# Performance work log

Hardware: AMD Instinct MI355X
Metric: run time of the kernel (lower is better)

Reference implementation:

```python
import jax, jax.numpy as jnp
import numpy as np

B, C, N = 4, 1, 1048576  # batch, channels (==spatial_dim==1), grid points
H = 32                   # correction_hidden
DX = 1.0                 # grid spacing


def setup_inputs() -> dict:
    key = jax.random.key(0)
    ks = jax.random.split(key, 4)
    u = jax.random.normal(ks[0], (B, C, N), dtype=jnp.float32)
    # correction MLP params (Linear 1->32, 32->32, 32->1). Original zero-inits
    # the last layer; we use small random values so the correction path is
    # numerically non-trivial for kernel correctness testing.
    W1 = jax.random.normal(ks[1], (1, H), dtype=jnp.float32) * 0.1
    b1 = jnp.zeros((H,), dtype=jnp.float32)
    W2 = jax.random.normal(ks[2], (H, H), dtype=jnp.float32) * 0.1
    b2 = jnp.zeros((H,), dtype=jnp.float32)
    W3 = jax.random.normal(ks[3], (H, 1), dtype=jnp.float32) * 0.1
    b3 = jnp.zeros((1,), dtype=jnp.float32)
    return dict(u=u, W1=W1, b1=b1, W2=W2, b2=b2, W3=W3, b3=b3)


def reference(u, W1, b1, W2, b2, W3, b3):
    # FD Laplacian via 1D stencil [1, -2, 1] with zero padding (== conv1d pad=1),
    # then / dx^2.  u: (B, C, N)
    up = jnp.pad(u, ((0, 0), (0, 0), (1, 1)))
    lap = (up[..., :-2] - 2.0 * u + up[..., 2:]) / (DX * DX)
    # correction MLP on per-point features (B, N, C)
    x = jnp.transpose(u, (0, 2, 1))           # (B, N, 1)
    h = jnp.tanh(x @ W1 + b1)                 # (B, N, 32)
    h = jnp.tanh(h @ W2 + b2)                 # (B, N, 32)
    corr = h @ W3 + b3                        # (B, N, 1)
    corr = jnp.transpose(corr, (0, 2, 1)).reshape(u.shape)  # (B, C, N)
    return lap + corr
```

## Files before the change

kernel.cpp:

```cpp
#include <hip/hip_runtime.h>
#include <hip/hip_bf16.h>
#include <math.h>

#define TBL_N       1024
#define TBL_LO      (-10.0f)
#define TBL_HI      (10.0f)
#define TBL_ENTRIES (TBL_N + 2)
#define ROW_N       1048576

__global__ __launch_bounds__(256)
void build_table(const float* __restrict__ c0, const float* __restrict__ c1,
                 const float* __restrict__ c2, const float* __restrict__ c3,
                 const float* __restrict__ W2, const float* __restrict__ b3,
                 float* __restrict__ tbl_g) {
    const int tid  = blockIdx.x * 256 + threadIdx.x;
    const int wave = tid >> 6;
    const int half = (threadIdx.x >> 5) & 1;
    const int j    = threadIdx.x & 31;

    const float a0 = c0[j], a1 = c1[j], a2 = c2[j], a3 = c3[j];
    const int m = (__ballot(a0 != 0.0f) ? 1 : 0) |
                  (__ballot(a1 != 0.0f) ? 2 : 0) |
                  (__ballot(a2 != 0.0f) ? 4 : 0) |
                  (__ballot(a3 != 0.0f) ? 8 : 0);
    float w1 = a0, bb1 = a1, bb2 = a2, w3 = a3;
    if (__popc(m) == 2) {
        const float cand[4] = {a0, a1, a2, a3};
        int f = 0; while (!((m >> f) & 1)) ++f;
        int s = f + 1; while (!((m >> s) & 1)) ++s;
        w1 = cand[f]; w3 = cand[s]; bb1 = 0.0f; bb2 = 0.0f;
    }

    const int e = wave * 2 + half;
    if (e >= TBL_ENTRIES) return;
    const int  en = (e > TBL_N) ? TBL_N : e;
    const float h = (TBL_HI - TBL_LO) / (float)TBL_N;
    const float x = TBL_LO + h * (float)en;

    float h1 = tanhf(fmaf(x, w1, bb1));

    float acc = bb2;
#pragma unroll
    for (int i = 0; i < 32; ++i)
        acc = fmaf(__shfl(h1, i, 32), W2[i * 32 + j], acc);

    float p = tanhf(acc) * w3;
#pragma unroll
    for (int off = 16; off; off >>= 1)
        p += __shfl_down(p, off, 32);

    if (j == 0) tbl_g[e] = p + b3[0];
}

__global__ __launch_bounds__(256)
void hybrid_main(const float* __restrict__ u, float* __restrict__ out,
                 const float* __restrict__ tbl_g, int total) {
    __shared__ float tbl[TBL_ENTRIES];
    for (int k = threadIdx.x; k < TBL_ENTRIES; k += 256)
        tbl[k] = tbl_g[k];
    __syncthreads();

    const float scale = (float)TBL_N / (TBL_HI - TBL_LO);
    const float bias  = -TBL_LO * scale;
    const float tmax  = (float)TBL_N - 0.001f;
    const int nch     = total >> 3;
    const int stride  = gridDim.x * blockDim.x;

    for (int c = blockIdx.x * blockDim.x + threadIdx.x; c < nch; c += stride) {
        const int g  = c << 3;
        const int i0 = g & (ROW_N - 1);
        const float4 p0 = *(const float4*)(u + g);
        const float4 p1 = *(const float4*)(u + g + 4);
        const float v[8] = {p0.x, p0.y, p0.z, p0.w, p1.x, p1.y, p1.z, p1.w};

        const bool atL = (i0 == 0);
        const bool atR = (i0 + 8 == ROW_N);
        float left  = u[atL ? g : g - 1];
        float right = u[atR ? g + 7 : g + 8];
        left  = atL ? 0.0f : left;
        right = atR ? 0.0f : right;

        float r[8];
#pragma unroll
        for (int k = 0; k < 8; ++k) {
            const float lm = (k == 0) ? left  : v[k - 1];
            const float rp = (k == 7) ? right : v[k + 1];
            float t = fmaf(v[k], scale, bias);
            t = fminf(fmaxf(t, 0.0f), tmax);
            const int   ki = (int)t;
            const float fr = t - (float)ki;
            const float f0 = tbl[ki];
            const float f1 = tbl[ki + 1];
            r[k] = (lm + rp) - 2.0f * v[k] + fmaf(f1 - f0, fr, f0);
        }

        *(float4*)(out + g)     = make_float4(r[0], r[1], r[2], r[3]);
        *(float4*)(out + g + 4) = make_float4(r[4], r[5], r[6], r[7]);
    }
}

extern "C" void kernel_launch(void* const* d_in, const int* in_sizes, int n_in,
                              void* d_out, int out_size, void* d_ws, size_t ws_size,
                              hipStream_t stream) {
    int n = (n_in > 0) ? n_in : 7;
    if (n > 7) n = 7;

    int iu = 0, ib3 = 0;
    for (int i = 1; i < n; ++i) {
        if (in_sizes[i] > in_sizes[iu])  iu  = i;
        if (in_sizes[i] < in_sizes[ib3]) ib3 = i;
    }
    int iw2 = -1;
    for (int i = 0; i < n; ++i) {
        if (i == iu || i == ib3) continue;
        if (iw2 < 0 || in_sizes[i] > in_sizes[iw2]) iw2 = i;
    }
    int rest[4], nr = 0;
    for (int i = 0; i < n && nr < 4; ++i) {
        if (i == iu || i == ib3 || i == iw2) continue;
        rest[nr++] = i;
    }

    const float* u  = (const float*)d_in[iu];
    const float* c0 = (const float*)d_in[rest[0]];
    const float* c1 = (const float*)d_in[rest[1]];
    const float* c2 = (const float*)d_in[rest[2]];
    const float* c3 = (const float*)d_in[rest[3]];
    const float* W2 = (const float*)d_in[iw2];
    const float* b3 = (const float*)d_in[ib3];

    float* out   = (float*)d_out;
    float* tbl_g = (float*)d_ws;
    (void)ws_size;

    const int waves   = (TBL_ENTRIES + 1) / 2;
    const int blocks1 = (waves * 64 + 255) / 256;
    build_table<<<blocks1, 256, 0, stream>>>(c0, c1, c2, c3, W2, b3, tbl_g);

    hybrid_main<<<1024, 256, 0, stream>>>(u, out, tbl_g, out_size);
}
```

Measured before the change: 83.99 us.

## Fuse table build into main kernel with per-block table and fast tanh

The separate table-building kernel and its global workspace round-trip are removed. Each block now evaluates the correction MLP for all table entries itself, using W2 staged in shared memory and an exp2/rcp-based tanh. The first two input chunks are loaded before the table build so their global-load latency overlaps with that compute. The trade is that table compute is repeated in every block, and the fast tanh may lose some accuracy.

```diff
diff --git a/kernel.cpp b/kernel.cpp
--- a/kernel.cpp
+++ b/kernel.cpp
@@ -1,5 +1,4 @@
 #include <hip/hip_runtime.h>
-#include <hip/hip_bf16.h>
 #include <math.h>
 
 #define TBL_N       1024
@@ -8,94 +7,170 @@
 #define TBL_ENTRIES (TBL_N + 2)
 #define ROW_N       1048576
 
-__global__ __launch_bounds__(256)
-void build_table(const float* __restrict__ c0, const float* __restrict__ c1,
-                 const float* __restrict__ c2, const float* __restrict__ c3,
-                 const float* __restrict__ W2, const float* __restrict__ b3,
-                 float* __restrict__ tbl_g) {
-    const int tid  = blockIdx.x * 256 + threadIdx.x;
-    const int wave = tid >> 6;
-    const int half = (threadIdx.x >> 5) & 1;
-    const int j    = threadIdx.x & 31;
-
-    const float a0 = c0[j], a1 = c1[j], a2 = c2[j], a3 = c3[j];
-    const int m = (__ballot(a0 != 0.0f) ? 1 : 0) |
-                  (__ballot(a1 != 0.0f) ? 2 : 0) |
-                  (__ballot(a2 != 0.0f) ? 4 : 0) |
-                  (__ballot(a3 != 0.0f) ? 8 : 0);
-    float w1 = a0, bb1 = a1, bb2 = a2, w3 = a3;
-    if (__popc(m) == 2) {
-        const float cand[4] = {a0, a1, a2, a3};
-        int f = 0; while (!((m >> f) & 1)) ++f;
-        int s = f + 1; while (!((m >> s) & 1)) ++s;
-        w1 = cand[f]; w3 = cand[s]; bb1 = 0.0f; bb2 = 0.0f;
-    }
-
-    const int e = wave * 2 + half;
-    if (e >= TBL_ENTRIES) return;
-    const int  en = (e > TBL_N) ? TBL_N : e;
-    const float h = (TBL_HI - TBL_LO) / (float)TBL_N;
-    const float x = TBL_LO + h * (float)en;
-
-    float h1 = tanhf(fmaf(x, w1, bb1));
-
-    float acc = bb2;
+__device__ __forceinline__ float tanh_fast(float x) {
+    const float e = __builtin_amdgcn_exp2f(x * 2.8853900817779268f);
+    return fmaf(-2.0f, __builtin_amdgcn_rcpf(e + 1.0f), 1.0f);
+}
+
+__device__ __forceinline__ float corr_eval(
+    float x, const float* __restrict__ pw1, const float* __restrict__ pb1,
+    const float* __restrict__ pb2, const float* __restrict__ pw3,
+    const float4 (*__restrict__ w2s4)[8], float bb3)
+{
+    float h1[32];
 #pragma unroll
     for (int i = 0; i < 32; ++i)
-        acc = fmaf(__shfl(h1, i, 32), W2[i * 32 + j], acc);
-
-    float p = tanhf(acc) * w3;
-#pragma unroll
-    for (int off = 16; off; off >>= 1)
-        p += __shfl_down(p, off, 32);
-
-    if (j == 0) tbl_g[e] = p + b3[0];
-}
-
-__global__ __launch_bounds__(256)
-void hybrid_main(const float* __restrict__ u, float* __restrict__ out,
-                 const float* __restrict__ tbl_g, int total) {
-    __shared__ float tbl[TBL_ENTRIES];
-    for (int k = threadIdx.x; k < TBL_ENTRIES; k += 256)
-        tbl[k] = tbl_g[k];
+        h1[i] = tanh_fast(fmaf(x, pw1[i], pb1[i]));
+    float r = 0.0f;
+    for (int j = 0; j < 32; ++j) {
+        float s = pb2[j];
+#pragma unroll
+        for (int i4 = 0; i4 < 8; ++i4) {
+            const float4 wv = w2s4[j][i4];
+            s = fmaf(h1[4 * i4 + 0], wv.x, s);
+            s = fmaf(h1[4 * i4 + 1], wv.y, s);
+            s = fmaf(h1[4 * i4 + 2], wv.z, s);
+            s = fmaf(h1[4 * i4 + 3], wv.w, s);
+        }
+        r = fmaf(tanh_fast(s), pw3[j], r);
+    }
+    return r + bb3;
+}
+
+__device__ __forceinline__ void process_chunk(
+    float* __restrict__ out, const float* __restrict__ tbl,
+    int g, float4 p0, float4 p1, float left, float right,
+    float scale, float bias, float tmax)
+{
+    const float v[8] = {p0.x, p0.y, p0.z, p0.w, p1.x, p1.y, p1.z, p1.w};
+    float r[8];
+#pragma unroll
+    for (int k = 0; k < 8; ++k) {
+        const float lm = (k == 0) ? left  : v[k - 1];
+        const float rp = (k == 7) ? right : v[k + 1];
+        float t = fmaf(v[k], scale, bias);
+        t = fminf(fmaxf(t, 0.0f), tmax);
+        const int   ki = (int)t;
+        const float fr = t - (float)ki;
+        const float f0 = tbl[ki];
+        const float f1 = tbl[ki + 1];
+        r[k] = (lm + rp) - 2.0f * v[k] + fmaf(f1 - f0, fr, f0);
+    }
+    *(float4*)(out + g)     = make_float4(r[0], r[1], r[2], r[3]);
+    *(float4*)(out + g + 4) = make_float4(r[4], r[5], r[6], r[7]);
+}
+
+__global__ __launch_bounds__(256, 4)
+void fused_hybrid(const float* __restrict__ u, float* __restrict__ out,
+                  const float* __restrict__ c0, const float* __restrict__ c1,
+                  const float* __restrict__ c2, const float* __restrict__ c3,
+                  const float* __restrict__ W2, const float* __restrict__ b3,
+                  int total)
+{
+    __shared__ float  tbl[TBL_ENTRIES];
+    __shared__ float4 w2s4[32][8];
+    __shared__ float  pw1[32], pb1[32], pb2[32], pw3[32];
+    __shared__ float  pb3s;
+
+    const int t   = threadIdx.x;
+    const int nch = total >> 3;
+    const int tpg = gridDim.x << 8;
+    const int cA  = (blockIdx.x << 8) + t;
+    const int cB  = cA + tpg;
+
+    float4 pa0 = {0, 0, 0, 0}, pa1 = {0, 0, 0, 0};
+    float  aL = 0.0f, aR = 0.0f;
+    const bool vA = cA < nch;
+    const int  gA = cA << 3;
+    if (vA) {
+        pa0 = *(const float4*)(u + gA);
+        pa1 = *(const float4*)(u + gA + 4);
+        const int  i0  = gA & (ROW_N - 1);
+        const bool atL = (i0 == 0);
+        const bool atR = (i0 + 8 == ROW_N);
+        const float l = u[atL ? gA : gA - 1];
+        const float r = u[atR ? gA + 7 : gA + 8];
+        aL = atL ? 0.0f : l;
+        aR = atR ? 0.0f : r;
+    }
+
+    {
+        const float4 w  = ((const float4*)W2)[t];
+        const int    i  = t >> 3;
+        const int    j0 = (t & 7) << 2;
+        float* w2f = (float*)w2s4;
+        w2f[(j0 + 0) * 32 + i] = w.x;
+        w2f[(j0 + 1) * 32 + i] = w.y;
+        w2f[(j0 + 2) * 32 + i] = w.z;
+        w2f[(j0 + 3) * 32 + i] = w.w;
+    }
+    if (t < 64) {
+        const int j = t & 31;
+        const float q0 = c0[j], q1 = c1[j], q2 = c2[j], q3 = c3[j];
+        const int m = (__ballot(q0 != 0.0f) ? 1 : 0) |
+                      (__ballot(q1 != 0.0f) ? 2 : 0) |
+                      (__ballot(q2 != 0.0f) ? 4 : 0) |
+                      (__ballot(q3 != 0.0f) ? 8 : 0);
+        float w1 = q0, bb1 = q1, bb2 = q2, w3 = q3;
+        if (__popc(m) == 2) {
+            const float cand[4] = {q0, q1, q2, q3};
+            int f = 0; while (!((m >> f) & 1)) ++f;
+            int s = f + 1; while (!((m >> s) & 1)) ++s;
+            w1 = cand[f]; w3 = cand[s]; bb1 = 0.0f; bb2 = 0.0f;
+        }
+        if (t < 32) { pw1[t] = w1; pb1[t] = bb1; pb2[t] = bb2; pw3[t] = w3; }
+        if (t == 0) pb3s = b3[0];
+    }
+    __syncthreads();
+
+    const float hstep = (TBL_HI - TBL_LO) / (float)TBL_N;
+    const float bb3   = pb3s;
+#pragma unroll
+    for (int q = 0; q < 4; ++q) {
+        const int e = t + q * 256;
+        const float x = fmaf(hstep, (float)e, TBL_LO);
+        tbl[e] = corr_eval(x, pw1, pb1, pb2, pw3, w2s4, bb3);
+    }
+    if (t < 2) {
+        tbl[1024 + t] = corr_eval(TBL_HI, pw1, pb1, pb2, pw3, w2s4, bb3);
+    }
     __syncthreads();
 
     const float scale = (float)TBL_N / (TBL_HI - TBL_LO);
     const float bias  = -TBL_LO * scale;
     const float tmax  = (float)TBL_N - 0.001f;
-    const int nch     = total >> 3;
-    const int stride  = gridDim.x * blockDim.x;
-
-    for (int c = blockIdx.x * blockDim.x + threadIdx.x; c < nch; c += stride) {
-        const int g  = c << 3;
-        const int i0 = g & (ROW_N - 1);
+
+    float4 pb0_ = {0, 0, 0, 0}, pb1_ = {0, 0, 0, 0};
+    float  bL = 0.0f, bR = 0.0f;
+    const bool vB = cB < nch;
+    const int  gB = cB << 3;
+    if (vB) {
+        pb0_ = *(const float4*)(u + gB);
+        pb1_ = *(const float4*)(u + gB + 4);
+        const int  i0  = gB & (ROW_N - 1);
+        const bool atL = (i0 == 0);
+        const bool atR = (i0 + 8 == ROW_N);
+        const float l = u[atL ? gB : gB - 1];
+        const float r = u[atR ? gB + 7 : gB + 8];
+        bL = atL ? 0.0f : l;
+        bR = atR ? 0.0f : r;
+    }
+
+    if (vA) process_chunk(out, tbl, gA, pa0, pa1, aL, aR, scale, bias, tmax);
+    if (vB) process_chunk(out, tbl, gB, pb0_, pb1_, bL, bR, scale, bias, tmax);
+
+    for (int c = cA + 2 * tpg; c < nch; c += tpg) {
+        const int g = c << 3;
         const float4 p0 = *(const float4*)(u + g);
         const float4 p1 = *(const float4*)(u + g + 4);
-        const float v[8] = {p0.x, p0.y, p0.z, p0.w, p1.x, p1.y, p1.z, p1.w};
-
+        const int  i0  = g & (ROW_N - 1);
         const bool atL = (i0 == 0);
         const bool atR = (i0 + 8 == ROW_N);
-        float left  = u[atL ? g : g - 1];
-        float right = u[atR ? g + 7 : g + 8];
-        left  = atL ? 0.0f : left;
-        right = atR ? 0.0f : right;
-
-        float r[8];
-#pragma unroll
-        for (int k = 0; k < 8; ++k) {
-            const float lm = (k == 0) ? left  : v[k - 1];
-            const float rp = (k == 7) ? right : v[k + 1];
-            float t = fmaf(v[k], scale, bias);
-            t = fminf(fmaxf(t, 0.0f), tmax);
-            const int   ki = (int)t;
-            const float fr = t - (float)ki;
-            const float f0 = tbl[ki];
-            const float f1 = tbl[ki + 1];
-            r[k] = (lm + rp) - 2.0f * v[k] + fmaf(f1 - f0, fr, f0);
-        }
-
-        *(float4*)(out + g)     = make_float4(r[0], r[1], r[2], r[3]);
-        *(float4*)(out + g + 4) = make_float4(r[4], r[5], r[6], r[7]);
+        float l = u[atL ? g : g - 1];
+        float r = u[atR ? g + 7 : g + 8];
+        l = atL ? 0.0f : l;
+        r = atR ? 0.0f : r;
+        process_chunk(out, tbl, g, p0, p1, l, r, scale, bias, tmax);
     }
 }
 
@@ -129,13 +204,9 @@
     const float* W2 = (const float*)d_in[iw2];
     const float* b3 = (const float*)d_in[ib3];
 
-    float* out   = (float*)d_out;
-    float* tbl_g = (float*)d_ws;
-    (void)ws_size;
-
-    const int waves   = (TBL_ENTRIES + 1) / 2;
-    const int blocks1 = (waves * 64 + 255) / 256;
-    build_table<<<blocks1, 256, 0, stream>>>(c0, c1, c2, c3, W2, b3, tbl_g);
-
-    hybrid_main<<<1024, 256, 0, stream>>>(u, out, tbl_g, out_size);
-}
+    float* out = (float*)d_out;
+    (void)d_ws; (void)ws_size;
+
+    fused_hybrid<<<1024, 256, 0, stream>>>(u, out, c0, c1, c2, c3, W2, b3,
+                                           out_size);
+}
```

Measured after the change: 134.3 us. +59.9%, slower.
